# Performance work log

Hardware: AMD Instinct MI355X
Metric: run time of the kernel (lower is better)

## Reference

```python
import jax, jax.numpy as jnp
import numpy as np
import math

NUM_ITER = 5
FEAT_STRIDE = 16
GAUSS_SIGMA = 1.0
HINGE_THRESHOLD = -999.0
MIN_FILTER_REG = 1e-3
ALPHA_EPS = 0.0


def apply_filter(feat, weights):
    # feat: (ni, ns, C, H, W); weights: (ns, C, fH, fW) -> scores (ni, ns, oH, oW)
    ni, ns, C, H, W = feat.shape
    fH, fW = weights.shape[-2], weights.shape[-1]
    x = feat.reshape(ni, ns * C, H, W)
    out = jax.lax.conv_general_dilated(
        x, weights, window_strides=(1, 1),
        padding=((fH // 2, fH // 2), (fW // 2, fW // 2)),
        dimension_numbers=('NCHW', 'OIHW', 'NCHW'),
        feature_group_count=ns)
    return out  # (ni, ns, oH, oW); oH = H + (fH+1)%2


def get_label(center, out_sz, sigma):
    # center: (ni, ns, 2) in (row, col) order
    k0 = jnp.arange(out_sz[0], dtype=jnp.float32)[None, None, :, None]
    k1 = jnp.arange(out_sz[1], dtype=jnp.float32)[None, None, None, :]
    g0 = jnp.exp(-0.5 / (sigma * sigma) * (k0 - center[..., 0][..., None, None]) ** 2)
    g1 = jnp.exp(-0.5 / (sigma * sigma) * (k1 - center[..., 1][..., None, None]) ** 2)
    return g0 * g1  # (ni, ns, oH, oW)


def _forward(weights, feat, bb, log_step_length, filter_reg):
    ni, ns = feat.shape[0], feat.shape[1]
    fH, fW = weights.shape[-2], weights.shape[-1]
    out_sz = (feat.shape[-2] + (fH + 1) % 2, feat.shape[-1] + (fW + 1) % 2)
    step = jnp.exp(log_step_length)[0]
    reg = jnp.maximum(filter_reg * filter_reg, MIN_FILTER_REG ** 2)[0]
    dmap_offset = jnp.array([fH % 2, fW % 2], jnp.float32) / 2.0
    # (x, y) -> (row, col), feature-grid coordinates
    center = ((bb[..., :2] + bb[..., 2:] / 2.0) / FEAT_STRIDE)[..., ::-1] - dmap_offset
    label = get_label(center, out_sz, GAUSS_SIGMA)
    mask = (label > HINGE_THRESHOLD).astype(feat.dtype)
    label = label * mask
    sw = math.sqrt(1.0 / ni)

    losses = []
    for _ in range(NUM_ITER):
        scores = apply_filter(feat, weights)
        scores_act = mask * scores + (1.0 - mask) * jax.nn.relu(scores)
        score_mask = mask + (1.0 - mask) * (jax.lax.stop_gradient(scores) > 0).astype(scores.dtype)
        residuals = sw * (scores_act - label)
        losses.append((jnp.sum(residuals ** 2) + reg * jnp.sum(weights ** 2)) / ns)
        residuals_mapped = score_mask * (sw * residuals)
        # feat-transpose = adjoint of apply_filter w.r.t. the filter weights
        _, vjp_fn = jax.vjp(lambda w: apply_filter(feat, w), weights)
        data_grad = vjp_fn(residuals_mapped)[0]
        weights_grad = data_grad + reg * weights
        scores_grad = apply_filter(feat, weights_grad)
        scores_grad = sw * (score_mask * scores_grad)
        alpha_num = jnp.sum(weights_grad ** 2, axis=(1, 2, 3))  # (ns,)
        alpha_den = jnp.maximum(
            jnp.sum(scores_grad.reshape(ni, ns, -1) ** 2, axis=(0, 2))
            + (reg + ALPHA_EPS) * alpha_num, 1e-8)
        alpha = alpha_num / alpha_den
        weights = weights - step * alpha[:, None, None, None] * weights_grad

    scores = apply_filter(feat, weights)
    scores = mask * scores + (1.0 - mask) * jax.nn.relu(scores)
    losses.append((jnp.sum((sw * (scores - label)) ** 2) + reg * jnp.sum(weights ** 2)) / ns)
    return weights, jnp.stack(losses)


def setup_inputs() -> dict:
    key = jax.random.key(0)
    k1, k2, k3, k4 = jax.random.split(key, 4)
    ni, ns, C, H, W, fH, fW = 3, 32, 512, 22, 22, 4, 4
    weights = 0.01 * jax.random.normal(k1, (ns, C, fH, fW), jnp.float32)
    feat = jax.random.normal(k2, (ni, ns, C, H, W), jnp.float32)
    # boxes (x, y, w, h) in image coords (image size = 22*16 = 352)
    xy = jax.random.uniform(k3, (ni, ns, 2), jnp.float32, 50.0, 250.0)
    wh = jax.random.uniform(k4, (ni, ns, 2), jnp.float32, 32.0, 96.0)
    bb = jnp.concatenate([xy, wh], axis=-1)
    log_step_length = jnp.zeros((1,), jnp.float32)  # log(1.0)
    filter_reg = 0.01 * jnp.ones((1,), jnp.float32)
    return {"weights": weights, "feat": feat, "bb": bb,
            "log_step_length": log_step_length, "filter_reg": filter_reg}


def reference(weights, feat, bb, log_step_length, filter_reg):
    return _forward(weights, feat, bb, log_step_length, filter_reg)
```

## Files before the change

### kernel.cpp

```cpp
#include <hip/hip_runtime.h>
#include <hip/hip_fp16.h>

#define NI 3
#define NS 32
#define CHN 512
#define OH 23
#define P2 529
#define NP 50784
#define UV 484
#define WSZ 262144

typedef unsigned int uint32;
typedef unsigned short u16;
typedef _Float16 h2 __attribute__((ext_vector_type(2)));
typedef _Float16 f16x8 __attribute__((ext_vector_type(8)));
typedef float f32x4 __attribute__((ext_vector_type(4)));

#define OFF_FEATT 0UL
#define OFF_LABEL 47579136UL
#define OFF_S0    47782272UL
#define OFF_S1    47985408UL
#define OFF_SGRAW 48188544UL
#define OFF_WG    48391680UL
#define OFF_WGF16 49440256UL
#define OFF_W0F16 49964544UL
#define OFF_PART  50488832UL

#define P_DEN   0
#define P_NUM   4320
#define P_LOSS  5600
#define P_WSQ0  5760
#define P_WSQA  5792
#define P_WSQ5  6816
#define P_L5    7840

__device__ __forceinline__ float waveSum(float v) {
#pragma unroll
  for (int o = 32; o > 0; o >>= 1) v += __shfl_xor(v, o, 64);
  return v;
}

__device__ __forceinline__ float alphaFor(const float* __restrict__ part, int t, int s,
                                          float reg) {
  const float* np_ = part + P_NUM + (size_t)(t * NS + s) * 8;
  const float* dp_ = part + P_DEN + (size_t)(t * NS + s) * 6;
  float nu = 0.f;
#pragma unroll
  for (int i = 0; i < 8; ++i) nu += np_[i];
  float de = 0.f;
#pragma unroll
  for (int i = 0; i < 6; ++i) de += dp_[i];
  return nu / fmaxf(de + reg * nu, 1e-8f);
}

__global__ __launch_bounds__(256) void k_setup(const float* __restrict__ feat,
                                               const float* __restrict__ w0,
                                               const float* __restrict__ bb,
                                               u16* __restrict__ featT,
                                               u16* __restrict__ w0f16,
                                               float* __restrict__ wmaster,
                                               float* __restrict__ label,
                                               float* __restrict__ part) {
  __shared__ float ldsT[7744];
  __shared__ float sred[4];
  int b = blockIdx.x, tid = threadIdx.x;
  if (b < 3072) {
    int snT = b >> 5, r5 = b & 31;
    int cb = r5 >> 2, uvq = r5 & 3;
    int s = snT / 3, n = snT % 3;
    const float* fsrc =
        feat + ((size_t)n * NS + s) * CHN * UV + (size_t)(cb * 64) * UV + uvq * 121;
#pragma unroll
    for (int it = 0; it < 31; ++it) {
      int idx = it * 256 + tid;
      if (idx < 7744) {
        int r = (unsigned)idx / 121u;
        int j = idx - r * 121;
        ldsT[idx] = fsrc[r * 484 + j];
      }
    }
    __syncthreads();
    uint32* dstb = (uint32*)featT +
                   ((size_t)(snT * 4 + (cb >> 1)) * UV + uvq * 121) * 64 + (cb & 1) * 32;
#pragma unroll
    for (int it = 0; it < 16; ++it) {
      int o = it * 256 + tid;
      if (o < 3872) {
        int uv = o >> 5, k = o & 31;
        float f0 = ldsT[(2 * k) * 121 + uv];
        float f1 = ldsT[(2 * k + 1) * 121 + uv];
        uint32 pk = (uint32)__half_as_ushort(__float2half(f0)) |
                    ((uint32)__half_as_ushort(__float2half(f1)) << 16);
        dstb[(size_t)uv * 64 + k] = pk;
      }
    }
  } else if (b < 3104) {
    int s = b - 3072;
    for (int i = tid; i < 8192; i += 256) {
      int tap = i >> 9, c = i & 511;
      w0f16[(size_t)s * 8192 + i] =
          __half_as_ushort(__float2half(w0[(size_t)s * 8192 + c * 16 + tap]));
    }
    float sq = 0.f;
    for (int i = tid; i < 8192; i += 256) {
      float v = w0[(size_t)s * 8192 + i];
      wmaster[(size_t)s * 8192 + i] = v;
      sq += v * v;
    }
    sq = waveSum(sq);
    if ((tid & 63) == 0) sred[tid >> 6] = sq;
    __syncthreads();
    if (tid == 0) part[P_WSQ0 + s] = sred[0] + sred[1] + sred[2] + sred[3];
  } else {
    int p = (b - 3104) * 256 + tid;
    if (p < NP) {
      int nsid = p / P2, rem = p % P2;
      int i = rem / OH, j = rem % OH;
      const float* bp = bb + (size_t)nsid * 4;
      float cr = (bp[1] + 0.5f * bp[3]) * 0.0625f;
      float cc = (bp[0] + 0.5f * bp[2]) * 0.0625f;
      float dy = (float)i - cr, dx = (float)j - cc;
      label[p] = __expf(-0.5f * (dy * dy + dx * dx));
    }
  }
}

__global__ __launch_bounds__(1024) void k_conv_fwd(const u16* __restrict__ featT,
                                                   const u16* __restrict__ wf16,
                                                   float* __restrict__ outbuf, int t,
                                                   float* __restrict__ part) {
  __shared__ uint32 w_lds[16 * 260];
  __shared__ float G[288 * 17];
  __shared__ float dred[16];
  int tid = threadIdx.x;
  int bidx = blockIdx.x;
  int snT = bidx >> 1, h = bidx & 1;
  int s = snT / 3, n = snT - s * 3;
  const uint32* wsrc = (const uint32*)(wf16 + (size_t)s * 8192);
  for (int i = tid; i < 4096; i += 1024) {
    int tap = i >> 8, p = i & 255;
    w_lds[tap * 260 + p] = wsrc[i];
  }
  __syncthreads();
  int wave = tid >> 6, lane = tid & 63;
  int q = lane >> 4, m16 = lane & 15;
  int uv0 = h ? 220 : 0;
  int ntiles = 18 - h;
  int t0 = wave;
  bool has2 = (wave + 16 < ntiles);
  int t1 = has2 ? wave + 16 : wave;
  f32x4 acc0 = {0.f, 0.f, 0.f, 0.f}, acc1 = {0.f, 0.f, 0.f, 0.f};
  size_t base = (size_t)snT * 4 * UV * 128;
  int r0i = uv0 + t0 * 16 + m16;
  if (r0i > 483) r0i = 483;
  int r1i = uv0 + t1 * 16 + m16;
  if (r1i > 483) r1i = 483;
  size_t row0 = (size_t)r0i * 128;
  size_t row1 = (size_t)r1i * 128;
#pragma unroll
  for (int step = 0; step < 16; ++step) {
    int cb = step >> 2, cin = (step & 3) * 32;
    size_t cbase = base + (size_t)cb * UV * 128 + cin + q * 8;
    f16x8 a0 = *(const f16x8*)(featT + cbase + row0);
    uint4 bw = *(const uint4*)&w_lds[m16 * 260 + step * 16 + q * 4];
    f16x8 bf = __builtin_bit_cast(f16x8, bw);
    acc0 = __builtin_amdgcn_mfma_f32_16x16x32_f16(a0, bf, acc0, 0, 0, 0);
    if (has2) {
      f16x8 a1 = *(const f16x8*)(featT + cbase + row1);
      acc1 = __builtin_amdgcn_mfma_f32_16x16x32_f16(a1, bf, acc1, 0, 0, 0);
    }
  }
#pragma unroll
  for (int r = 0; r < 4; ++r) G[(t0 * 16 + q * 4 + r) * 17 + m16] = acc0[r];
  if (has2) {
#pragma unroll
    for (int r = 0; r < 4; ++r) G[(t1 * 16 + q * 4 + r) * 17 + m16] = acc1[r];
  }
  __syncthreads();
  float dsq = 0.f;
  int y0 = h ? 12 : 0;
  int npix = h ? 253 : 276;
  int p = tid;
  if (p < npix) {
    int yl = p / 23, x = p - yl * 23;
    int y = y0 + yl;
    float val = 0.f;
#pragma unroll
    for (int ky = 0; ky < 4; ++ky) {
      int u = y + ky - 2;
      if ((unsigned)u < 22u) {
#pragma unroll
        for (int kx = 0; kx < 4; ++kx) {
          int v = x + kx - 2;
          if ((unsigned)v < 22u) val += G[(u * 22 + v - uv0) * 17 + ky * 4 + kx];
        }
      }
    }
    outbuf[(size_t)(n * NS + s) * P2 + y * 23 + x] = val;
    dsq = val * val;
  }
  if (t >= 0) {
    dsq = waveSum(dsq);
    if (lane == 0) dred[wave] = dsq;
    __syncthreads();
    if (tid == 0) {
      float dsum = 0.f;
#pragma unroll
      for (int i = 0; i < 16; ++i) dsum += dred[i];
      part[P_DEN + ((size_t)(t * NS + s) * 3 + n) * 2 + h] = dsum * (1.0f / 3.0f);
    }
  }
}

__global__ __launch_bounds__(768) void k_adjoint(
    int t, const u16* __restrict__ featT, const float* __restrict__ label,
    const float* __restrict__ scores_old, float* __restrict__ scores_new,
    const float* __restrict__ sgraw, float* __restrict__ wg, u16* __restrict__ wgf16,
    float* __restrict__ wmaster, float* __restrict__ part, const float* __restrict__ lsl,
    const float* __restrict__ fr) {
  __shared__ float r_lds[1950];
  __shared__ float red[12288];
  __shared__ float lred[12];
  __shared__ float nred2[2], wred2[2];
  int tid = threadIdx.x;
  int s = blockIdx.x >> 3, chunk = blockIdx.x & 7;
  int c0 = chunk * 64;
  int cp = tid & 31, tg1 = (tid >> 5) & 1, m = tid >> 6;
  int n = m >> 2, uq = m & 3;
  int u0 = (uq * 22) >> 2, u1 = ((uq + 1) * 22) >> 2;
  float step = __expf(lsl[0]);
  float frv = fr[0];
  float reg = fmaxf(frv * frv, 1e-6f);
  float alpha_p = (t >= 1) ? alphaFor(part, t - 1, s, reg) : 0.f;
  for (int i = tid; i < 1950; i += 768) r_lds[i] = 0.f;
  __syncthreads();
  float lsum = 0.f;
  for (int pl = tid; pl < 1587; pl += 768) {
    int nn = pl / P2, rem = pl % P2;
    int y = rem / OH, x = rem % OH;
    size_t gp = (size_t)(nn * NS + s) * P2 + rem;
    float S = scores_old[gp];
    if (t >= 1) S -= step * alpha_p * sgraw[gp];
    float d = S - label[gp];
    r_lds[nn * 650 + (y + 1) * 26 + (x + 1)] = d * (1.0f / 3.0f);
    if (chunk == 0) {
      if (t >= 1) scores_new[gp] = S;
      lsum += d * d;
    }
  }
  lsum = waveSum(lsum);
  if ((tid & 63) == 0) lred[tid >> 6] = lsum;
  __syncthreads();
  if (chunk == 0 && tid == 0) {
    float L = 0.f;
#pragma unroll
    for (int i = 0; i < 12; ++i) L += lred[i];
    part[P_LOSS + t * NS + s] = L * (1.0f / 3.0f);
  }
  const uint32* fb = (const uint32*)featT +
                     ((size_t)(s * 3 + n) * 4 + (chunk >> 1)) * UV * 64 +
                     (chunk & 1) * 32 + cp;
  float ac[16];
#pragma unroll
  for (int i = 0; i < 16; ++i) ac[i] = 0.f;
  const float* rbase = r_lds + n * 650;
  for (int u = u0; u < u1; ++u) {
    const float* rA = rbase + (u + 3 - tg1) * 26;
    const float* rB = rbase + (u + 1 - tg1) * 26;
    const uint32* fp_ = fb + (size_t)u * 22 * 64;
#pragma unroll
    for (int v = 0; v < 22; ++v) {
      uint32 fv = fp_[(size_t)v * 64];
      h2 hv = __builtin_bit_cast(h2, fv);
      float f0 = (float)hv[0], f1 = (float)hv[1];
#pragma unroll
      for (int kx = 0; kx < 4; ++kx) {
        float ra = rA[v + 3 - kx];
        float rb_ = rB[v + 3 - kx];
        ac[0 + kx] = fmaf(f0, ra, ac[0 + kx]);
        ac[4 + kx] = fmaf(f0, rb_, ac[4 + kx]);
        ac[8 + kx] = fmaf(f1, ra, ac[8 + kx]);
        ac[12 + kx] = fmaf(f1, rb_, ac[12 + kx]);
      }
    }
  }
#pragma unroll
  for (int cj = 0; cj < 2; ++cj)
#pragma unroll
    for (int kyi = 0; kyi < 2; ++kyi)
#pragma unroll
      for (int kx = 0; kx < 4; ++kx) {
        int ky = tg1 + 2 * kyi;
        int j = (cj * 4 + ky) * 4 + kx;
        red[(j * 12 + m) * 32 + cp] = ac[cj * 8 + kyi * 4 + kx];
      }
  __syncthreads();
  if (tid < 128) {
    int ocp = tid & 31, ky = tid >> 5;
    float wsq_part = 0.f, num_part = 0.f;
#pragma unroll
    for (int jj = 0; jj < 8; ++jj) {
      int cj = jj >> 2, kx = jj & 3;
      int j = (cj * 4 + ky) * 4 + kx;
      float dg = 0.f;
#pragma unroll
      for (int mm = 0; mm < 12; ++mm) dg += red[(j * 12 + mm) * 32 + ocp];
      int c = c0 + 2 * ocp + cj;
      int tap = ky * 4 + kx;
      size_t widx = (size_t)s * 8192 + (size_t)c * 16 + tap;
      float wold = wmaster[widx];
      float wnew = wold;
      if (t >= 1) {
        wnew = wold - step * alpha_p * wg[widx];
        wmaster[widx] = wnew;
      }
      float wgn = dg + reg * wnew;
      wg[widx] = wgn;
      wgf16[(size_t)s * 8192 + tap * 512 + c] = __half_as_ushort(__float2half(wgn));
      wsq_part += wnew * wnew;
      num_part += wgn * wgn;
    }
    wsq_part = waveSum(wsq_part);
    num_part = waveSum(num_part);
    if ((tid & 63) == 0) {
      nred2[tid >> 6] = num_part;
      wred2[tid >> 6] = wsq_part;
    }
  }
  __syncthreads();
  if (tid == 0) {
    part[P_NUM + (size_t)(t * NS + s) * 8 + chunk] = nred2[0] + nred2[1];
    if (t >= 1) part[P_WSQA + (size_t)((t - 1) * NS + s) * 8 + chunk] = wred2[0] + wred2[1];
  }
}

__global__ void k_final(float* __restrict__ wmaster, const float* __restrict__ wg,
                        const float* __restrict__ scores4, const float* __restrict__ sgraw,
                        const float* __restrict__ label, float* __restrict__ part,
                        const float* __restrict__ lsl, const float* __restrict__ fr) {
  __shared__ float alpha_s[32];
  __shared__ float red4[4];
  int b = blockIdx.x, tid = threadIdx.x;
  float step = __expf(lsl[0]);
  float frv = fr[0];
  float reg = fmaxf(frv * frv, 1e-6f);
  if (tid < 32) alpha_s[tid] = alphaFor(part, 4, tid, reg);
  __syncthreads();
  if (b < 1024) {
    int idx = b * 256 + tid;
    int s = idx >> 13;
    float w5 = wmaster[idx] - step * alpha_s[s] * wg[idx];
    wmaster[idx] = w5;
    float sq = waveSum(w5 * w5);
    if ((tid & 63) == 0) red4[tid >> 6] = sq;
    __syncthreads();
    if (tid == 0) part[P_WSQ5 + b] = red4[0] + red4[1] + red4[2] + red4[3];
  } else {
    int p = (b - 1024) * 256 + tid;
    float contrib = 0.f;
    if (p < NP) {
      int nsid = p / P2;
      int s = nsid & 31;
      float s5 = scores4[p] - step * alpha_s[s] * sgraw[p];
      float d = s5 - label[p];
      contrib = d * d;
    }
    contrib = waveSum(contrib);
    if ((tid & 63) == 0) red4[tid >> 6] = contrib;
    __syncthreads();
    if (tid == 0)
      part[P_L5 + (b - 1024)] = (red4[0] + red4[1] + red4[2] + red4[3]) * (1.0f / 3.0f);
  }
}

__global__ void k_losses(float* __restrict__ out_losses, const float* __restrict__ part,
                         const float* __restrict__ fr) {
  __shared__ float red[8];
  int tid = threadIdx.x;
  float frv = fr[0];
  float reg = fmaxf(frv * frv, 1e-6f);
  float v5 = 0.f;
  for (int i = tid; i < 1024; i += 256) v5 += part[P_WSQ5 + i];
  v5 = waveSum(v5);
  if ((tid & 63) == 0) red[tid >> 6] = v5;
  __syncthreads();
  float wsq5 = red[0] + red[1] + red[2] + red[3];
  float l5 = 0.f;
  for (int i = tid; i < 199; i += 256) l5 += part[P_L5 + i];
  l5 = waveSum(l5);
  if ((tid & 63) == 0) red[4 + (tid >> 6)] = l5;
  __syncthreads();
  float loss5 = red[4] + red[5] + red[6] + red[7];
  if (tid < 5) {
    int t = tid;
    float ls = 0.f;
    for (int i = 0; i < 32; ++i) ls += part[P_LOSS + t * NS + i];
    float ws_ = 0.f;
    if (t == 0) {
      for (int i = 0; i < 32; ++i) ws_ += part[P_WSQ0 + i];
    } else {
      for (int i = 0; i < 256; ++i) ws_ += part[P_WSQA + (t - 1) * 256 + i];
    }
    out_losses[t] = (ls + reg * ws_) * (1.0f / 32.0f);
  }
  if (tid == 5) out_losses[5] = (loss5 + reg * wsq5) * (1.0f / 32.0f);
}

extern "C" void kernel_launch(void* const* d_in, const int* in_sizes, int n_in,
                              void* d_out, int out_size, void* d_ws, size_t ws_size,
                              hipStream_t stream) {
  const float* w0 = (const float*)d_in[0];
  const float* feat = (const float*)d_in[1];
  const float* bb = (const float*)d_in[2];
  const float* lsl = (const float*)d_in[3];
  const float* fr = (const float*)d_in[4];
  float* out = (float*)d_out;
  char* ws = (char*)d_ws;
  u16* featT = (u16*)(ws + OFF_FEATT);
  float* label = (float*)(ws + OFF_LABEL);
  float* s0 = (float*)(ws + OFF_S0);
  float* s1 = (float*)(ws + OFF_S1);
  float* sgraw = (float*)(ws + OFF_SGRAW);
  float* wg = (float*)(ws + OFF_WG);
  u16* wgf16 = (u16*)(ws + OFF_WGF16);
  u16* w0f16 = (u16*)(ws + OFF_W0F16);
  float* part = (float*)(ws + OFF_PART);

  k_setup<<<3303, 256, 0, stream>>>(feat, w0, bb, featT, w0f16, out, label, part);
  k_conv_fwd<<<192, 1024, 0, stream>>>(featT, w0f16, s0, -1, part);
  float* sbuf[2] = {s0, s1};
  for (int t = 0; t < 5; ++t) {
    const float* so = (t == 0) ? s0 : sbuf[(t - 1) & 1];
    float* sn = sbuf[t & 1];
    k_adjoint<<<256, 768, 0, stream>>>(t, featT, label, so, sn, sgraw, wg, wgf16, out, part,
                                       lsl, fr);
    k_conv_fwd<<<192, 1024, 0, stream>>>(featT, wgf16, sgraw, t, part);
  }
  k_final<<<1223, 256, 0, stream>>>(out, wg, s0, sgraw, label, part, lsl, fr);
  k_losses<<<1, 256, 0, stream>>>(out + WSZ, part, fr);
}
```

Before: 376.2 us.

## Compute adjoint weight gradient with MFMA GEMM over channel-major fp16 features

Setup now also writes a second fp16 copy of the features laid out channel-major with K = image×spatial (padded to 512 per image). The adjoint kernel builds a shifted residual matrix per filter tap in LDS and computes the weight gradient as a 16×16×32 fp16 MFMA GEMM split across two K halves, replacing the scalar FMA loop and its large LDS reduction. This trades extra setup bandwidth and workspace for matrix-core throughput, and it also quantizes the residuals to fp16, which may cost accuracy.

Result: slower. 389.7 us (+3.6%).

```diff
diff --git a/kernel.cpp b/kernel.cpp
--- a/kernel.cpp
+++ b/kernel.cpp
@@ -9,6 +9,8 @@
 #define NP 50784
 #define UV 484
 #define WSZ 262144
+#define KTOT 1536
+#define RSP 1544
 
 typedef unsigned int uint32;
 typedef unsigned short u16;
@@ -25,6 +27,7 @@
 #define OFF_WGF16 49440256UL
 #define OFF_W0F16 49964544UL
 #define OFF_PART  50488832UL
+#define OFF_FEATC 50521600UL
 
 #define P_DEN   0
 #define P_NUM   4320
@@ -57,6 +60,7 @@
                                                const float* __restrict__ w0,
                                                const float* __restrict__ bb,
                                                u16* __restrict__ featT,
+                                               u16* __restrict__ featC,
                                                u16* __restrict__ w0f16,
                                                float* __restrict__ wmaster,
                                                float* __restrict__ label,
@@ -92,6 +96,24 @@
         uint32 pk = (uint32)__half_as_ushort(__float2half(f0)) |
                     ((uint32)__half_as_ushort(__float2half(f1)) << 16);
         dstb[(size_t)uv * 64 + k] = pk;
+      }
+    }
+    u16* fcbase = featC + ((size_t)(s * CHN + cb * 64)) * KTOT + n * 512 + uvq * 121;
+#pragma unroll
+    for (int it = 0; it < 31; ++it) {
+      int idx = it * 256 + tid;
+      if (idx < 7744) {
+        int r = (unsigned)idx / 121u;
+        int j = idx - r * 121;
+        fcbase[(size_t)r * KTOT + j] = __half_as_ushort(__float2half(ldsT[r * 121 + j]));
+      }
+    }
+    if (uvq == 3) {
+      u16* fpbase = featC + ((size_t)(s * CHN + cb * 64)) * KTOT + n * 512 + 484;
+      for (int idx = tid; idx < 64 * 28; idx += 256) {
+        int r = (unsigned)idx / 28u;
+        int j = idx - r * 28;
+        fpbase[(size_t)r * KTOT + j] = 0;
       }
     }
   } else if (b < 3104) {
@@ -212,37 +234,33 @@
   }
 }
 
-__global__ __launch_bounds__(768) void k_adjoint(
-    int t, const u16* __restrict__ featT, const float* __restrict__ label,
+__global__ __launch_bounds__(512) void k_adjoint(
+    int t, const u16* __restrict__ featC, const float* __restrict__ label,
     const float* __restrict__ scores_old, float* __restrict__ scores_new,
     const float* __restrict__ sgraw, float* __restrict__ wg, u16* __restrict__ wgf16,
     float* __restrict__ wmaster, float* __restrict__ part, const float* __restrict__ lsl,
     const float* __restrict__ fr) {
-  __shared__ float r_lds[1950];
-  __shared__ float red[12288];
-  __shared__ float lred[12];
-  __shared__ float nred2[2], wred2[2];
+  __shared__ float r_lds[3 * P2];
+  __shared__ __align__(16) u16 rs[16 * RSP];
+  __shared__ __align__(16) float kred[4][64][4];
+  __shared__ float lred[8], nred8[8], wred8[8];
   int tid = threadIdx.x;
   int s = blockIdx.x >> 3, chunk = blockIdx.x & 7;
   int c0 = chunk * 64;
-  int cp = tid & 31, tg1 = (tid >> 5) & 1, m = tid >> 6;
-  int n = m >> 2, uq = m & 3;
-  int u0 = (uq * 22) >> 2, u1 = ((uq + 1) * 22) >> 2;
   float step = __expf(lsl[0]);
   float frv = fr[0];
   float reg = fmaxf(frv * frv, 1e-6f);
   float alpha_p = (t >= 1) ? alphaFor(part, t - 1, s, reg) : 0.f;
-  for (int i = tid; i < 1950; i += 768) r_lds[i] = 0.f;
-  __syncthreads();
+
   float lsum = 0.f;
-  for (int pl = tid; pl < 1587; pl += 768) {
-    int nn = pl / P2, rem = pl % P2;
-    int y = rem / OH, x = rem % OH;
+  for (int pl = tid; pl < 1587; pl += 512) {
+    int nn = (unsigned)pl / (unsigned)P2;
+    int rem = pl - nn * P2;
     size_t gp = (size_t)(nn * NS + s) * P2 + rem;
     float S = scores_old[gp];
     if (t >= 1) S -= step * alpha_p * sgraw[gp];
     float d = S - label[gp];
-    r_lds[nn * 650 + (y + 1) * 26 + (x + 1)] = d * (1.0f / 3.0f);
+    r_lds[nn * P2 + rem] = d * (1.0f / 3.0f);
     if (chunk == 0) {
       if (t >= 1) scores_new[gp] = S;
       lsum += d * d;
@@ -254,83 +272,85 @@
   if (chunk == 0 && tid == 0) {
     float L = 0.f;
 #pragma unroll
-    for (int i = 0; i < 12; ++i) L += lred[i];
+    for (int i = 0; i < 8; ++i) L += lred[i];
     part[P_LOSS + t * NS + s] = L * (1.0f / 3.0f);
   }
-  const uint32* fb = (const uint32*)featT +
-                     ((size_t)(s * 3 + n) * 4 + (chunk >> 1)) * UV * 64 +
-                     (chunk & 1) * 32 + cp;
-  float ac[16];
-#pragma unroll
-  for (int i = 0; i < 16; ++i) ac[i] = 0.f;
-  const float* rbase = r_lds + n * 650;
-  for (int u = u0; u < u1; ++u) {
-    const float* rA = rbase + (u + 3 - tg1) * 26;
-    const float* rB = rbase + (u + 1 - tg1) * 26;
-    const uint32* fp_ = fb + (size_t)u * 22 * 64;
-#pragma unroll
-    for (int v = 0; v < 22; ++v) {
-      uint32 fv = fp_[(size_t)v * 64];
-      h2 hv = __builtin_bit_cast(h2, fv);
-      float f0 = (float)hv[0], f1 = (float)hv[1];
-#pragma unroll
-      for (int kx = 0; kx < 4; ++kx) {
-        float ra = rA[v + 3 - kx];
-        float rb_ = rB[v + 3 - kx];
-        ac[0 + kx] = fmaf(f0, ra, ac[0 + kx]);
-        ac[4 + kx] = fmaf(f0, rb_, ac[4 + kx]);
-        ac[8 + kx] = fmaf(f1, ra, ac[8 + kx]);
-        ac[12 + kx] = fmaf(f1, rb_, ac[12 + kx]);
-      }
-    }
-  }
-#pragma unroll
-  for (int cj = 0; cj < 2; ++cj)
-#pragma unroll
-    for (int kyi = 0; kyi < 2; ++kyi)
-#pragma unroll
-      for (int kx = 0; kx < 4; ++kx) {
-        int ky = tg1 + 2 * kyi;
-        int j = (cj * 4 + ky) * 4 + kx;
-        red[(j * 12 + m) * 32 + cp] = ac[cj * 8 + kyi * 4 + kx];
-      }
-  __syncthreads();
-  if (tid < 128) {
-    int ocp = tid & 31, ky = tid >> 5;
-    float wsq_part = 0.f, num_part = 0.f;
-#pragma unroll
-    for (int jj = 0; jj < 8; ++jj) {
-      int cj = jj >> 2, kx = jj & 3;
-      int j = (cj * 4 + ky) * 4 + kx;
-      float dg = 0.f;
-#pragma unroll
-      for (int mm = 0; mm < 12; ++mm) dg += red[(j * 12 + mm) * 32 + ocp];
-      int c = c0 + 2 * ocp + cj;
-      int tap = ky * 4 + kx;
-      size_t widx = (size_t)s * 8192 + (size_t)c * 16 + tap;
+
+  for (int idx = tid; idx < 16 * RSP; idx += 512) {
+    int tap = (unsigned)idx / (unsigned)RSP;
+    int k = idx - tap * RSP;
+    float val = 0.f;
+    if (k < KTOT) {
+      int n = k >> 9, uv = k & 511;
+      if (uv < UV) {
+        int u = (unsigned)uv / 22u;
+        int v = uv - u * 22;
+        int ky = tap >> 2, kx = tap & 3;
+        int y = u + 2 - ky, x = v + 2 - kx;
+        if ((unsigned)y < 23u && (unsigned)x < 23u) val = r_lds[n * P2 + y * OH + x];
+      }
+    }
+    rs[idx] = __half_as_ushort(__float2half(val));
+  }
+  __syncthreads();
+
+  int wave = tid >> 6, lane = tid & 63;
+  int q = lane >> 4, m16 = lane & 15;
+  int tile = wave & 3, khalf = wave >> 2;
+  int c = c0 + tile * 16 + m16;
+  const u16* arow = featC + ((size_t)(s * CHN + c)) * KTOT + khalf * 768 + q * 8;
+  const u16* brow = rs + m16 * RSP + khalf * 768 + q * 8;
+  f32x4 acc = {0.f, 0.f, 0.f, 0.f};
+#pragma unroll
+  for (int ks = 0; ks < 24; ++ks) {
+    f16x8 a = *(const f16x8*)(arow + ks * 32);
+    f16x8 bf = *(const f16x8*)(brow + ks * 32);
+    acc = __builtin_amdgcn_mfma_f32_16x16x32_f16(a, bf, acc, 0, 0, 0);
+  }
+  if (khalf == 1) *(f32x4*)&kred[tile][lane][0] = acc;
+  __syncthreads();
+
+  float num_part = 0.f, wsq_part = 0.f;
+  if (khalf == 0) {
+    f32x4 o = *(const f32x4*)&kred[tile][lane][0];
+    acc += o;
+    int tap = m16;
+    int ccb = c0 + tile * 16 + q * 4;
+    union { u16 h[4]; uint2 v2; } pk;
+#pragma unroll
+    for (int r = 0; r < 4; ++r) {
+      int cc = ccb + r;
+      size_t widx = (size_t)s * 8192 + (size_t)cc * 16 + tap;
       float wold = wmaster[widx];
       float wnew = wold;
       if (t >= 1) {
         wnew = wold - step * alpha_p * wg[widx];
         wmaster[widx] = wnew;
       }
-      float wgn = dg + reg * wnew;
+      float wgn = acc[r] + reg * wnew;
       wg[widx] = wgn;
-      wgf16[(size_t)s * 8192 + tap * 512 + c] = __half_as_ushort(__float2half(wgn));
+      pk.h[r] = __half_as_ushort(__float2half(wgn));
       wsq_part += wnew * wnew;
       num_part += wgn * wgn;
     }
-    wsq_part = waveSum(wsq_part);
-    num_part = waveSum(num_part);
-    if ((tid & 63) == 0) {
-      nred2[tid >> 6] = num_part;
-      wred2[tid >> 6] = wsq_part;
-    }
+    *(uint2*)&wgf16[(size_t)s * 8192 + (size_t)tap * 512 + ccb] = pk.v2;
+  }
+  num_part = waveSum(num_part);
+  wsq_part = waveSum(wsq_part);
+  if (lane == 0) {
+    nred8[wave] = num_part;
+    wred8[wave] = wsq_part;
   }
   __syncthreads();
   if (tid == 0) {
-    part[P_NUM + (size_t)(t * NS + s) * 8 + chunk] = nred2[0] + nred2[1];
-    if (t >= 1) part[P_WSQA + (size_t)((t - 1) * NS + s) * 8 + chunk] = wred2[0] + wred2[1];
+    float nsum = 0.f, wsum = 0.f;
+#pragma unroll
+    for (int i = 0; i < 8; ++i) {
+      nsum += nred8[i];
+      wsum += wred8[i];
+    }
+    part[P_NUM + (size_t)(t * NS + s) * 8 + chunk] = nsum;
+    if (t >= 1) part[P_WSQA + (size_t)((t - 1) * NS + s) * 8 + chunk] = wsum;
   }
 }
 
@@ -425,14 +445,15 @@
   u16* wgf16 = (u16*)(ws + OFF_WGF16);
   u16* w0f16 = (u16*)(ws + OFF_W0F16);
   float* part = (float*)(ws + OFF_PART);
-
-  k_setup<<<3303, 256, 0, stream>>>(feat, w0, bb, featT, w0f16, out, label, part);
+  u16* featC = (u16*)(ws + OFF_FEATC);
+
+  k_setup<<<3303, 256, 0, stream>>>(feat, w0, bb, featT, featC, w0f16, out, label, part);
   k_conv_fwd<<<192, 1024, 0, stream>>>(featT, w0f16, s0, -1, part);
   float* sbuf[2] = {s0, s1};
   for (int t = 0; t < 5; ++t) {
     const float* so = (t == 0) ? s0 : sbuf[(t - 1) & 1];
     float* sn = sbuf[t & 1];
-    k_adjoint<<<256, 768, 0, stream>>>(t, featT, label, so, sn, sgraw, wg, wgf16, out, part,
+    k_adjoint<<<256, 512, 0, stream>>>(t, featC, label, so, sn, sgraw, wg, wgf16, out, part,
                                        lsl, fr);
     k_conv_fwd<<<192, 1024, 0, stream>>>(featT, wgf16, sgraw, t, part);
   }
```
